# Kernel optimization log

Hardware: AMD Instinct MI355X
Metric: run time of the kernel (lower is better)

## Reference

```python
import jax, jax.numpy as jnp
import numpy as np

P = 8  # patch size hardcoded in FSAS/DFFN
EPS = 1e-5


def conv1x1(x, w):
    # x: [B,C,H,W], w: [Cout,Cin]
    return jnp.einsum('bchw,oc->bohw', x, w)


def dwconv3(x, w):
    # depthwise 3x3, w: [C,1,3,3]
    return jax.lax.conv_general_dilated(
        x, w, window_strides=(1, 1), padding='SAME',
        dimension_numbers=('NCHW', 'OIHW', 'NCHW'),
        feature_group_count=x.shape[1])


def layernorm_c(x, w, b):
    # WithBias LayerNorm over channel dim (torch: b c h w -> b (h w) c, LN over c)
    mu = jnp.mean(x, axis=1, keepdims=True)
    var = jnp.var(x, axis=1, keepdims=True)
    return (x - mu) / jnp.sqrt(var + EPS) * w[None, :, None, None] + b[None, :, None, None]


def to_patches(x):
    # [B,C,H,W] -> [B,C,H/P,W/P,P,P]
    B, C, H, W = x.shape
    return x.reshape(B, C, H // P, P, W // P, P).transpose(0, 1, 2, 4, 3, 5)


def from_patches(xp):
    B, C, h, w, p1, p2 = xp.shape
    return xp.transpose(0, 1, 2, 4, 3, 5).reshape(B, C, h * p1, w * p2)


def fsas(x, w_hidden, dw, norm_w, norm_b, w_out):
    hidden = conv1x1(x, w_hidden)          # [B,6d,H,W]
    qkv = dwconv3(hidden, dw)
    q, k, v = jnp.split(qkv, 3, axis=1)    # each [B,2d,H,W]
    qf = jnp.fft.rfft2(to_patches(q))
    kf = jnp.fft.rfft2(to_patches(k))
    out = jnp.fft.irfft2(qf * kf, s=(P, P))
    out = layernorm_c(from_patches(out), norm_w, norm_b)
    return conv1x1(v * out, w_out)


def dffn(x, w_in, fft_w, dw, w_out):
    x = conv1x1(x, w_in)                   # [B,2h,H,W]
    xf = jnp.fft.rfft2(to_patches(x))
    # fft_w: [2h,1,1,P,P//2+1] broadcasts against [B,2h,h,w,P,P//2+1]
    x = from_patches(jnp.fft.irfft2(xf * fft_w, s=(P, P)))
    x1, x2 = jnp.split(dwconv3(x, dw), 2, axis=1)
    return conv1x1(jax.nn.gelu(x1, approximate=False) * x2, w_out)


def setup_inputs() -> dict:
    key = jax.random.key(0)
    ks = jax.random.split(key, 10)
    d = 48
    h = int(d * 3)  # ffn_expansion_factor=3 -> hidden_features=144
    B, H, W = 2, 256, 256

    def n(k, shape, s=0.05):
        return jax.random.normal(k, shape, jnp.float32) * s

    return {
        'x': jax.random.normal(ks[0], (B, d, H, W), jnp.float32),
        'norm1_w': jnp.ones((d,), jnp.float32),
        'norm1_b': jnp.zeros((d,), jnp.float32),
        'attn_w_hidden': n(ks[1], (6 * d, d)),
        'attn_dw': n(ks[2], (6 * d, 1, 3, 3), 0.2),
        'attn_norm_w': jnp.ones((2 * d,), jnp.float32),
        'attn_norm_b': jnp.zeros((2 * d,), jnp.float32),
        'attn_w_out': n(ks[3], (d, 2 * d)),
        'norm2_w': jnp.ones((d,), jnp.float32),
        'norm2_b': jnp.zeros((d,), jnp.float32),
        'ffn_w_in': n(ks[4], (2 * h, d)),
        'ffn_fft': 1.0 + n(ks[5], (2 * h, 1, 1, P, P // 2 + 1), 0.1),
        'ffn_dw': n(ks[6], (2 * h, 1, 3, 3), 0.2),
        'ffn_w_out': n(ks[7], (d, h)),
    }


def reference(x, norm1_w, norm1_b, attn_w_hidden, attn_dw, attn_norm_w,
              attn_norm_b, attn_w_out, norm2_w, norm2_b, ffn_w_in, ffn_fft,
              ffn_dw, ffn_w_out):
    x = x + fsas(layernorm_c(x, norm1_w, norm1_b),
                 attn_w_hidden, attn_dw, attn_norm_w, attn_norm_b, attn_w_out)
    x = x + dffn(layernorm_c(x, norm2_w, norm2_b),
                 ffn_w_in, ffn_fft, ffn_dw, ffn_w_out)
    return x
```

## Files before the change

### kernel.cpp

```cpp
#include <hip/hip_runtime.h>
#include <hip/hip_bf16.h>
#include <cstddef>


constexpr int HWC = 65536;

typedef short short8 __attribute__((ext_vector_type(8)));
typedef __bf16 bf16x8 __attribute__((ext_vector_type(8)));
typedef float f32x4 __attribute__((ext_vector_type(4)));

__device__ inline unsigned short f2bf(float f) {
  __hip_bfloat16 h = __float2bfloat16(f);
  return *reinterpret_cast<unsigned short*>(&h);
}
__device__ inline float bf2f(unsigned short u) {
  __hip_bfloat16 h;
  *reinterpret_cast<unsigned short*>(&h) = u;
  return __bfloat162float(h);
}

union V8 { uint4 v; unsigned short us[8]; short s[8]; };

__device__ inline void load8f(const unsigned short* p, float* f) {
  V8 u; u.v = *reinterpret_cast<const uint4*>(p);
#pragma unroll
  for (int j = 0; j < 8; j++) f[j] = bf2f(u.us[j]);
}
__device__ inline void store8bf(unsigned short* p, const float* f) {
  V8 u;
#pragma unroll
  for (int j = 0; j < 8; j++) u.us[j] = f2bf(f[j]);
  *reinterpret_cast<uint4*>(p) = u.v;
}

__device__ inline void fdft8(const float* x, float* e) {
  const float c = 0.70710678118654752f;
  float t0 = x[0] + x[4], t1 = x[0] - x[4];
  float t2 = x[2] + x[6], t3 = x[2] - x[6];
  float t4 = x[1] + x[5], t5 = x[1] - x[5];
  float t6 = x[3] + x[7], t7 = x[3] - x[7];
  float A = c * (t5 - t7), B = c * (t5 + t7);
  float s1 = t0 + t2, s2 = t4 + t6;
  e[0] = s1 + s2;
  e[7] = s1 - s2;
  e[1] = t1 + A;
  e[5] = t1 - A;
  e[2] = -(B + t3);
  e[6] = t3 - B;
  e[3] = t0 - t2;
  e[4] = t6 - t4;
}

__global__ __launch_bounds__(64) void k_prep_w(
    const float* __restrict__ awh, const float* __restrict__ awo,
    const float* __restrict__ fwi, const float* __restrict__ fwo,
    unsigned short* __restrict__ wp) {
  int row = blockIdx.x, t = threadIdx.x;
  const float* src; int K, KP; unsigned short* dst;
  if (row < 288)      { src = awh + row * 48;        K = 48;  KP = 64;
                        dst = wp + row * 64; }
  else if (row < 336) { int r = row - 288; src = awo + r * 96; K = 96; KP = 96;
                        dst = wp + 18432 + r * 96; }
  else if (row < 624) { int r = row - 336; src = fwi + r * 48; K = 48; KP = 64;
                        dst = wp + 23040 + r * 64; }
  else                { int r = row - 624; src = fwo + r * 144; K = 144; KP = 160;
                        dst = wp + 41472 + r * 160; }
  for (int k = t; k < KP; k += 64) dst[k] = f2bf(k < K ? src[k] : 0.f);
}

template <int M, int K, int KP, int XF, int EPI>
__global__ __launch_bounds__(256) void k_gemm(
    const unsigned short* __restrict__ wb, const void* __restrict__ s1,
    const unsigned short* __restrict__ s2, const float* __restrict__ lnw,
    const float* __restrict__ lnb, const void* __restrict__ res,
    void* __restrict__ out) {
  constexpr int STRIDE = KP + 8;
  constexpr int KS = KP / 32;
  constexpr int NT = (M + 63) / 64;
  __shared__ __align__(16) short Xs[64 * STRIDE];
  __shared__ __align__(16) short Vs[(XF == 2) ? 64 * STRIDE : 4];
  __shared__ float redS[4][64], redS2[4][64], mus[64], invs[64];

  int tid = threadIdx.x;
  unsigned bid = blockIdx.x;
  int b = (int)(bid >> 10);
  int hw0 = (int)(bid & 1023) * 64;

  if (XF == 1) {
    const float* xp = (const float*)s1 + (size_t)b * 48 * HWC + hw0;
    for (int idx = tid; idx < 48 * 16; idx += 256) {
      int c = idx >> 4, colg = (idx & 15) * 4;
      float4 f = *reinterpret_cast<const float4*>(xp + (size_t)c * HWC + colg);
      Xs[(colg + 0) * STRIDE + c] = (short)f2bf(f.x);
      Xs[(colg + 1) * STRIDE + c] = (short)f2bf(f.y);
      Xs[(colg + 2) * STRIDE + c] = (short)f2bf(f.z);
      Xs[(colg + 3) * STRIDE + c] = (short)f2bf(f.w);
    }
  } else if (XF == 2) {
    const unsigned short* up =
        (const unsigned short*)s1 + (size_t)b * 96 * HWC + hw0;
    const unsigned short* vp = s2 + ((size_t)(b * 288 + 192)) * HWC + hw0;
    for (int idx = tid; idx < 96 * 16; idx += 256) {
      int c = idx >> 4, colg = (idx & 15) * 4;
      ushort4 uv = *reinterpret_cast<const ushort4*>(up + (size_t)c * HWC + colg);
      Xs[(colg + 0) * STRIDE + c] = (short)uv.x;
      Xs[(colg + 1) * STRIDE + c] = (short)uv.y;
      Xs[(colg + 2) * STRIDE + c] = (short)uv.z;
      Xs[(colg + 3) * STRIDE + c] = (short)uv.w;
      ushort4 vv = *reinterpret_cast<const ushort4*>(vp + (size_t)c * HWC + colg);
      Vs[(colg + 0) * STRIDE + c] = (short)vv.x;
      Vs[(colg + 1) * STRIDE + c] = (short)vv.y;
      Vs[(colg + 2) * STRIDE + c] = (short)vv.z;
      Vs[(colg + 3) * STRIDE + c] = (short)vv.w;
    }
  } else if (XF == 3) {
    const unsigned short* xp =
        (const unsigned short*)s1 + (size_t)b * 48 * HWC + hw0;
    for (int idx = tid; idx < 48 * 16; idx += 256) {
      int c = idx >> 4, colg = (idx & 15) * 4;
      ushort4 uv = *reinterpret_cast<const ushort4*>(xp + (size_t)c * HWC + colg);
      Xs[(colg + 0) * STRIDE + c] = (short)uv.x;
      Xs[(colg + 1) * STRIDE + c] = (short)uv.y;
      Xs[(colg + 2) * STRIDE + c] = (short)uv.z;
      Xs[(colg + 3) * STRIDE + c] = (short)uv.w;
    }
  } else {
    const unsigned short* p1 =
        (const unsigned short*)s1 + (size_t)b * 96 * HWC + hw0;
    const unsigned short* p2 = s2 + (size_t)b * 48 * HWC + hw0;
    for (int idx = tid; idx < K * 16; idx += 256) {
      int c = idx >> 4, colg = (idx & 15) * 4;
      const unsigned short* p =
          (c < 96) ? (p1 + (size_t)c * HWC + colg)
                   : (p2 + (size_t)(c - 96) * HWC + colg);
      ushort4 uv = *reinterpret_cast<const ushort4*>(p);
      Xs[(colg + 0) * STRIDE + c] = (short)uv.x;
      Xs[(colg + 1) * STRIDE + c] = (short)uv.y;
      Xs[(colg + 2) * STRIDE + c] = (short)uv.z;
      Xs[(colg + 3) * STRIDE + c] = (short)uv.w;
    }
  }

  if constexpr (KP > K) {
    constexpr int PAD = KP - K;
    for (int idx = tid; idx < 64 * PAD; idx += 256) {
      int col = idx / PAD, c = K + (idx % PAD);
      Xs[col * STRIDE + c] = 0;
    }
  }

  if (XF != 0) {
    constexpr int KC = (XF == 2) ? 96 : 48;
    __syncthreads();
    {
      int col = tid & 63, q = tid >> 6;
      float s = 0.f, s2 = 0.f;
      for (int c = q * (KC / 4); c < (q + 1) * (KC / 4); c++) {
        float v = bf2f((unsigned short)Xs[col * STRIDE + c]);
        s += v; s2 += v * v;
      }
      redS[q][col] = s; redS2[q][col] = s2;
    }
    __syncthreads();
    if (tid < 64) {
      float ss = redS[0][tid] + redS[1][tid] + redS[2][tid] + redS[3][tid];
      float ss2 = redS2[0][tid] + redS2[1][tid] + redS2[2][tid] + redS2[3][tid];
      float mu = ss * (1.f / KC);
      float var = ss2 * (1.f / KC) - mu * mu;
      mus[tid] = mu; invs[tid] = rsqrtf(var + 1e-5f);
    }
    __syncthreads();
    for (int idx = tid; idx < KC * 64; idx += 256) {
      int c = idx >> 6, col = idx & 63;
      float v = bf2f((unsigned short)Xs[col * STRIDE + c]);
      v = (v - mus[col]) * invs[col] * lnw[c] + lnb[c];
      if (XF == 2) v *= bf2f((unsigned short)Vs[col * STRIDE + c]);
      Xs[col * STRIDE + c] = (short)f2bf(v);
    }
  }
  __syncthreads();

  int lane = tid & 63, wvi = tid >> 6;
  int quad = lane >> 4, mc = lane & 15;
  int kbase = quad * 8;

  short8 bfr[4][KS];
#pragma unroll
  for (int ns = 0; ns < 4; ns++)
#pragma unroll
    for (int ks = 0; ks < KS; ks++)
      bfr[ns][ks] = *reinterpret_cast<const short8*>(
          Xs + (ns * 16 + mc) * STRIDE + ks * 32 + kbase);

  short* Es = Xs;
#pragma unroll
  for (int t = 0; t < NT; t++) {
    int mb = (wvi + 4 * t) * 16;
    f32x4 accs[4];
    if (mb < M) {
      short8 afr[KS];
#pragma unroll
      for (int ks = 0; ks < KS; ks++)
        afr[ks] = *reinterpret_cast<const short8*>(
            wb + (size_t)(mb + mc) * KP + ks * 32 + kbase);
#pragma unroll
      for (int ns = 0; ns < 4; ns++) {
        f32x4 acc = {0.f, 0.f, 0.f, 0.f};
#pragma unroll
        for (int ks = 0; ks < KS; ks++)
          acc = __builtin_amdgcn_mfma_f32_16x16x32_bf16(
              __builtin_bit_cast(bf16x8, afr[ks]),
              __builtin_bit_cast(bf16x8, bfr[ns][ks]), acc, 0, 0, 0);
        accs[ns] = acc;
      }
    }
    __syncthreads();
    if (mb < M) {
      int chl = wvi * 16 + quad * 4;
#pragma unroll
      for (int ns = 0; ns < 4; ns++)
#pragma unroll
        for (int r = 0; r < 4; r++)
          Es[(chl + r) * 72 + ns * 16 + mc] = (short)f2bf(accs[ns][r]);
    }
    __syncthreads();
#pragma unroll
    for (int i = 0; i < 2; i++) {
      int chl = (tid >> 3) + 32 * i;
      int px0 = (tid & 7) * 8;
      int m = 64 * t + chl;
      if (m < M) {
        V8 ev;
        ev.v = *reinterpret_cast<const uint4*>(Es + chl * 72 + px0);
        size_t off = ((size_t)(b * ((EPI == 0) ? M : 48) + m)) * HWC + hw0 + px0;
        if (EPI == 0) {
          *reinterpret_cast<uint4*>((unsigned short*)out + off) = ev.v;
        } else if (EPI == 1) {
          const float* rp = (const float*)res + off;
          float4 ra = *reinterpret_cast<const float4*>(rp);
          float4 rb = *reinterpret_cast<const float4*>(rp + 4);
          V8 pk;
          pk.us[0] = f2bf(ra.x + bf2f(ev.us[0]));
          pk.us[1] = f2bf(ra.y + bf2f(ev.us[1]));
          pk.us[2] = f2bf(ra.z + bf2f(ev.us[2]));
          pk.us[3] = f2bf(ra.w + bf2f(ev.us[3]));
          pk.us[4] = f2bf(rb.x + bf2f(ev.us[4]));
          pk.us[5] = f2bf(rb.y + bf2f(ev.us[5]));
          pk.us[6] = f2bf(rb.z + bf2f(ev.us[6]));
          pk.us[7] = f2bf(rb.w + bf2f(ev.us[7]));
          *reinterpret_cast<uint4*>((unsigned short*)out + off) = pk.v;
        } else {
          V8 rv;
          rv.v = *reinterpret_cast<const uint4*>((const unsigned short*)res + off);
          float* op = (float*)out + off;
          float4 oa, ob;
          oa.x = bf2f(rv.us[0]) + bf2f(ev.us[0]);
          oa.y = bf2f(rv.us[1]) + bf2f(ev.us[1]);
          oa.z = bf2f(rv.us[2]) + bf2f(ev.us[2]);
          oa.w = bf2f(rv.us[3]) + bf2f(ev.us[3]);
          ob.x = bf2f(rv.us[4]) + bf2f(ev.us[4]);
          ob.y = bf2f(rv.us[5]) + bf2f(ev.us[5]);
          ob.z = bf2f(rv.us[6]) + bf2f(ev.us[6]);
          ob.w = bf2f(rv.us[7]) + bf2f(ev.us[7]);
          *reinterpret_cast<float4*>(op) = oa;
          *reinterpret_cast<float4*>(op + 4) = ob;
        }
      }
    }
  }
}

__global__ __launch_bounds__(256) void k_dwconv3v(
    const unsigned short* __restrict__ in, const float* __restrict__ dw,
    unsigned short* __restrict__ out) {
  int tid = threadIdx.x;
  unsigned bid = blockIdx.x;
  int y0 = (int)(bid & 31) * 8;
  unsigned t = bid >> 5;
  int c = 192 + (int)(t % 96u);
  int b = (int)(t / 96u);
  const unsigned short* ip = in + ((size_t)(b * 288 + c)) * HWC;
  float wv[9];
#pragma unroll
  for (int k = 0; k < 9; k++) wv[k] = dw[c * 9 + k];
  int r = tid >> 5, seg = tid & 31, lane = tid & 63;
  int y = y0 + r;
  float f[3][8];
#pragma unroll
  for (int dy = 0; dy < 3; dy++) {
    int yy = y + dy - 1;
    if (yy >= 0 && yy < 256) {
      load8f(ip + yy * 256 + seg * 8, f[dy]);
    } else {
#pragma unroll
      for (int j = 0; j < 8; j++) f[dy][j] = 0.f;
    }
  }
  float o[8];
#pragma unroll
  for (int dy = 0; dy < 3; dy++) {
    float lv = __shfl(f[dy][7], lane - 1, 64);
    float rv = __shfl(f[dy][0], lane + 1, 64);
    if (seg == 0) lv = 0.f;
    if (seg == 31) rv = 0.f;
#pragma unroll
    for (int j = 0; j < 8; j++) {
      float xl = (j == 0) ? lv : f[dy][j - 1];
      float xr = (j == 7) ? rv : f[dy][j + 1];
      float v = xl * wv[dy * 3] + f[dy][j] * wv[dy * 3 + 1] + xr * wv[dy * 3 + 2];
      o[j] = (dy == 0) ? v : o[j] + v;
    }
  }
  store8bf(out + ((size_t)(b * 288 + c)) * HWC + y * 256 + seg * 8, o);
}

__global__ __launch_bounds__(256) void k_fsas_fused(
    const unsigned short* __restrict__ hid, const float* __restrict__ dw,
    unsigned short* __restrict__ out) {
  constexpr int LSTR = 260;
  __shared__ __align__(16) float qs[8 * LSTR];
  __shared__ __align__(16) float kt[8 * LSTR];
  int tid = threadIdx.x;
  unsigned bid = blockIdx.x;
  int py = (int)(bid & 31);
  int c = (int)((bid >> 5) % 96u);
  int b = (int)((bid >> 5) / 96u);
  const unsigned short* qp = hid + ((size_t)(b * 288 + c)) * HWC;
  const unsigned short* kp = hid + ((size_t)(b * 288 + 96 + c)) * HWC;
  float w1[9], w2[9];
#pragma unroll
  for (int k = 0; k < 9; k++) {
    w1[k] = dw[c * 9 + k];
    w2[k] = dw[(96 + c) * 9 + k];
  }
  int r = tid >> 5, seg = tid & 31, lane = tid & 63;
  int y = py * 8 + r;
  float f1[3][8], f2[3][8];
#pragma unroll
  for (int dy = 0; dy < 3; dy++) {
    int yy = y + dy - 1;
    if (yy >= 0 && yy < 256) {
      load8f(qp + yy * 256 + seg * 8, f1[dy]);
      load8f(kp + yy * 256 + seg * 8, f2[dy]);
    } else {
#pragma unroll
      for (int j = 0; j < 8; j++) { f1[dy][j] = 0.f; f2[dy][j] = 0.f; }
    }
  }
  float d1[8], d2[8];
#pragma unroll
  for (int j = 0; j < 8; j++) { d1[j] = 0.f; d2[j] = 0.f; }
#pragma unroll
  for (int dy = 0; dy < 3; dy++) {
    float lv1 = __shfl(f1[dy][7], lane - 1, 64);
    float rv1 = __shfl(f1[dy][0], lane + 1, 64);
    float lv2 = __shfl(f2[dy][7], lane - 1, 64);
    float rv2 = __shfl(f2[dy][0], lane + 1, 64);
    if (seg == 0) { lv1 = 0.f; lv2 = 0.f; }
    if (seg == 31) { rv1 = 0.f; rv2 = 0.f; }
#pragma unroll
    for (int j = 0; j < 8; j++) {
      float xl1 = (j == 0) ? lv1 : f1[dy][j - 1];
      float xr1 = (j == 7) ? rv1 : f1[dy][j + 1];
      float xl2 = (j == 0) ? lv2 : f2[dy][j - 1];
      float xr2 = (j == 7) ? rv2 : f2[dy][j + 1];
      d1[j] += xl1 * w1[dy * 3] + f1[dy][j] * w1[dy * 3 + 1] + xr1 * w1[dy * 3 + 2];
      d2[j] += xl2 * w2[dy * 3] + f2[dy][j] * w2[dy * 3 + 1] + xr2 * w2[dy * 3 + 2];
    }
  }
  {
    float e1[8], e2[8];
    fdft8(d1, e1);
    fdft8(d2, e2);
    float4 a1 = {e1[0], e1[1], e1[2], e1[3]};
    float4 b1 = {e1[4], e1[5], e1[6], e1[7]};
    float4 a2 = {e2[0], e2[1], e2[2], e2[3]};
    float4 b2 = {e2[4], e2[5], e2[6], e2[7]};
    *reinterpret_cast<float4*>(&qs[r * LSTR + seg * 8]) = a1;
    *reinterpret_cast<float4*>(&qs[r * LSTR + seg * 8 + 4]) = b1;
    *reinterpret_cast<float4*>(&kt[r * LSTR + seg * 8]) = a2;
    *reinterpret_cast<float4*>(&kt[r * LSTR + seg * 8 + 4]) = b2;
  }
  __syncthreads();
  int p = tid >> 3, a = tid & 7;
  float Z[8];
#pragma unroll
  for (int j = 0; j < 8; j++) Z[j] = 0.f;
#pragma unroll
  for (int i = 0; i < 8; i++) {
    float4 qa = *reinterpret_cast<const float4*>(&qs[i * LSTR + p * 8]);
    float4 qb = *reinterpret_cast<const float4*>(&qs[i * LSTR + p * 8 + 4]);
    int ar = (a - i) & 7;
    float4 ka = *reinterpret_cast<const float4*>(&kt[ar * LSTR + p * 8]);
    float4 kb = *reinterpret_cast<const float4*>(&kt[ar * LSTR + p * 8 + 4]);
    Z[0] += qa.x * ka.x;
    Z[7] += qb.w * kb.w;
    Z[1] += qa.y * ka.y - qa.z * ka.z;
    Z[2] += qa.y * ka.z + qa.z * ka.y;
    Z[3] += qa.w * ka.w - qb.x * kb.x;
    Z[4] += qa.w * kb.x + qb.x * ka.w;
    Z[5] += qb.y * kb.y - qb.z * kb.z;
    Z[6] += qb.y * kb.z + qb.z * kb.y;
  }
  float acc[8];
  {
    const float c2 = 0.70710678118654752f;
    float Z0 = Z[0], Z1r = Z[1], Z1i = Z[2], Z2r = Z[3];
    float Z2i = Z[4], Z3r = Z[5], Z3i = Z[6], Z4 = Z[7];
    float u0 = Z0 + Z4, u1 = Z0 - Z4;
    float E = 2.f * Z2r, F = 2.f * (Z1r + Z3r), G = 2.f * (Z1i - Z3i);
    float T = 2.f * Z2i;
    float P = 2.f * c2 * (Z1r - Z1i), Qv = 2.f * c2 * (Z1r + Z1i);
    float R = 2.f * c2 * (Z3r + Z3i), S = 2.f * c2 * (Z3r - Z3i);
    acc[0] = 0.125f * (u0 + E + F);
    acc[4] = 0.125f * (u0 + E - F);
    acc[2] = 0.125f * (u0 - E - G);
    acc[6] = 0.125f * (u0 - E + G);
    acc[1] = 0.125f * (u1 + P - T - R);
    acc[3] = 0.125f * (u1 - Qv + T + S);
    acc[5] = 0.125f * (u1 - P - T + R);
    acc[7] = 0.125f * (u1 + Qv + T - S);
  }
  store8bf(out + ((size_t)(b * 96 + c)) * HWC + (py * 8 + a) * 256 + p * 8,
           acc);
}

__device__ const float c_cos8[8] = {
    1.f, 0.70710678118654752f, 0.f, -0.70710678118654752f,
    -1.f, -0.70710678118654752f, 0.f, 0.70710678118654752f};

__global__ __launch_bounds__(64) void k_make_cmat(
    const float* __restrict__ fftw, unsigned short* __restrict__ cmat) {
  __shared__ float sf[64];
  int c = blockIdx.x;
  int a = threadIdx.x >> 3, b2 = threadIdx.x & 7;
  const float* W = fftw + c * 40;
  float acc = 0.f;
  for (int u = 0; u < 8; u++) {
    for (int v = 0; v < 8; v++) {
      float wv;
      if (v <= 4) {
        if (v == 0 || v == 4)
          wv = 0.5f * (W[u * 5 + v] + W[((8 - u) & 7) * 5 + v]);
        else
          wv = W[u * 5 + v];
      } else {
        wv = W[((8 - u) & 7) * 5 + (8 - v)];
      }
      acc += wv * c_cos8[(u * a + v * b2) & 7];
    }
  }
  sf[threadIdx.x] = acc * (1.f / 64.f);
  __syncthreads();
  unsigned short* cp = cmat + (size_t)c * 4096 + threadIdx.x * 64;
  for (int k8 = 0; k8 < 64; k8 += 8) {
    float v[8];
    int ka = k8 >> 3;
    int ia = ((a - ka) & 7) * 8;
#pragma unroll
    for (int j = 0; j < 8; j++) v[j] = sf[ia + ((b2 - j) & 7)];
    store8bf(cp + k8, v);
  }
}

__global__ __launch_bounds__(256) void k_patchconv_mfma(
    unsigned short* y, const unsigned short* __restrict__ cmat) {
  __shared__ __align__(16) short Bs[32 * 72];
  __shared__ __align__(16) short As[64 * 72];
  int tid = threadIdx.x;
  unsigned bid = blockIdx.x;
  int py = (int)(bid & 31);
  int c = (int)((bid >> 5) % 288u);
  int b = (int)((bid >> 5) / 288u);
  unsigned short* yp = y + ((size_t)(b * 288 + c)) * HWC + py * 2048;
  {
    int rr = tid >> 5, seg = tid & 31;
    *reinterpret_cast<uint4*>(Bs + seg * 72 + rr * 8) =
        *reinterpret_cast<const uint4*>(yp + rr * 256 + seg * 8);
  }
  {
    const unsigned short* cp = cmat + (size_t)c * 4096;
    int m = tid >> 2, kq = (tid & 3) * 16;
    *reinterpret_cast<uint4*>(As + m * 72 + kq) =
        *reinterpret_cast<const uint4*>(cp + m * 64 + kq);
    *reinterpret_cast<uint4*>(As + m * 72 + kq + 8) =
        *reinterpret_cast<const uint4*>(cp + m * 64 + kq + 8);
  }
  __syncthreads();
  int lane = tid & 63, wvi = tid >> 6;
  int quad = lane >> 4, mc = lane & 15;
  int kbase = quad * 8;
  short8 afr[2];
#pragma unroll
  for (int ks = 0; ks < 2; ks++)
    afr[ks] = *reinterpret_cast<const short8*>(
        As + (wvi * 16 + mc) * 72 + ks * 32 + kbase);
#pragma unroll
  for (int nt = 0; nt < 2; nt++) {
    short8 bfr[2];
#pragma unroll
    for (int ks = 0; ks < 2; ks++)
      bfr[ks] = *reinterpret_cast<const short8*>(
          Bs + (nt * 16 + mc) * 72 + ks * 32 + kbase);
    f32x4 acc = {0.f, 0.f, 0.f, 0.f};
#pragma unroll
    for (int ks = 0; ks < 2; ks++)
      acc = __builtin_amdgcn_mfma_f32_16x16x32_bf16(
          __builtin_bit_cast(bf16x8, afr[ks]),
          __builtin_bit_cast(bf16x8, bfr[ks]), acc, 0, 0, 0);
    int p = nt * 16 + mc;
    int m0 = wvi * 16 + quad * 4;
    int a = m0 >> 3, b8 = m0 & 7;
    ushort4 pk;
    pk.x = f2bf(acc[0]); pk.y = f2bf(acc[1]);
    pk.z = f2bf(acc[2]); pk.w = f2bf(acc[3]);
    *reinterpret_cast<ushort4*>(yp + a * 256 + p * 8 + b8) = pk;
  }
}

__global__ __launch_bounds__(256) void k_ffn_gate(
    const unsigned short* __restrict__ z, const float* __restrict__ dwf,
    unsigned short* __restrict__ g1, unsigned short* __restrict__ g2) {
  int tid = threadIdx.x;
  unsigned bid = blockIdx.x;
  int y0 = (int)(bid & 31) * 8;
  unsigned t = bid >> 5;
  int c = (int)(t % 144u);
  int b = (int)(t / 144u);
  const unsigned short* zp1 = z + ((size_t)(b * 288 + c)) * HWC;
  const unsigned short* zp2 = z + ((size_t)(b * 288 + 144 + c)) * HWC;
  float w1[9], w2[9];
#pragma unroll
  for (int k = 0; k < 9; k++) {
    w1[k] = dwf[c * 9 + k];
    w2[k] = dwf[(144 + c) * 9 + k];
  }
  int r = tid >> 5, seg = tid & 31, lane = tid & 63;
  int y = y0 + r;
  float f1[3][8], f2[3][8];
#pragma unroll
  for (int dy = 0; dy < 3; dy++) {
    int yy = y + dy - 1;
    if (yy >= 0 && yy < 256) {
      load8f(zp1 + yy * 256 + seg * 8, f1[dy]);
      load8f(zp2 + yy * 256 + seg * 8, f2[dy]);
    } else {
#pragma unroll
      for (int j = 0; j < 8; j++) { f1[dy][j] = 0.f; f2[dy][j] = 0.f; }
    }
  }
  float d1[8], d2[8];
#pragma unroll
  for (int j = 0; j < 8; j++) { d1[j] = 0.f; d2[j] = 0.f; }
#pragma unroll
  for (int dy = 0; dy < 3; dy++) {
    float lv1 = __shfl(f1[dy][7], lane - 1, 64);
    float rv1 = __shfl(f1[dy][0], lane + 1, 64);
    float lv2 = __shfl(f2[dy][7], lane - 1, 64);
    float rv2 = __shfl(f2[dy][0], lane + 1, 64);
    if (seg == 0) { lv1 = 0.f; lv2 = 0.f; }
    if (seg == 31) { rv1 = 0.f; rv2 = 0.f; }
#pragma unroll
    for (int j = 0; j < 8; j++) {
      float xl1 = (j == 0) ? lv1 : f1[dy][j - 1];
      float xr1 = (j == 7) ? rv1 : f1[dy][j + 1];
      float xl2 = (j == 0) ? lv2 : f2[dy][j - 1];
      float xr2 = (j == 7) ? rv2 : f2[dy][j + 1];
      d1[j] += xl1 * w1[dy * 3] + f1[dy][j] * w1[dy * 3 + 1] + xr1 * w1[dy * 3 + 2];
      d2[j] += xl2 * w2[dy * 3] + f2[dy][j] * w2[dy * 3 + 1] + xr2 * w2[dy * 3 + 2];
    }
  }
  float o[8];
#pragma unroll
  for (int j = 0; j < 8; j++)
    o[j] = 0.5f * d1[j] * (1.f + erff(d1[j] * 0.70710678118654752f)) * d2[j];
  unsigned short* gp = (c < 96)
      ? g1 + ((size_t)(b * 96 + c)) * HWC
      : g2 + ((size_t)(b * 48 + (c - 96))) * HWC;
  store8bf(gp + y * 256 + seg * 8, o);
}

extern "C" void kernel_launch(void* const* d_in, const int* in_sizes, int n_in,
                              void* d_out, int out_size, void* d_ws,
                              size_t ws_size, hipStream_t stream) {
  (void)in_sizes; (void)n_in; (void)out_size; (void)ws_size;
  const float* x   = (const float*)d_in[0];
  const float* n1w = (const float*)d_in[1];
  const float* n1b = (const float*)d_in[2];
  const float* awh = (const float*)d_in[3];
  const float* adw = (const float*)d_in[4];
  const float* anw = (const float*)d_in[5];
  const float* anb = (const float*)d_in[6];
  const float* awo = (const float*)d_in[7];
  const float* n2w = (const float*)d_in[8];
  const float* n2b = (const float*)d_in[9];
  const float* fwi = (const float*)d_in[10];
  const float* fff = (const float*)d_in[11];
  const float* fdw = (const float*)d_in[12];
  const float* fwo = (const float*)d_in[13];

  unsigned short* QKV  = (unsigned short*)d_ws;
  unsigned short* HID  = (unsigned short*)((char*)d_ws + 75497472);
  unsigned short* U    = (unsigned short*)((char*)d_ws + 150994944);
  unsigned short* X1   = (unsigned short*)((char*)d_ws + 176160768);
  unsigned short* G2   = (unsigned short*)((char*)d_ws + 188743680);
  unsigned short* CMAT = G2;
  unsigned short* WP   = (unsigned short*)((char*)d_ws + 201326592);
  unsigned short* WA = WP;
  unsigned short* WO = WP + 18432;
  unsigned short* WI = WP + 23040;
  unsigned short* WF = WP + 41472;

  k_prep_w<<<672, 64, 0, stream>>>(awh, awo, fwi, fwo, WP);
  k_make_cmat<<<288, 64, 0, stream>>>(fff, CMAT);
  k_gemm<288, 48, 64, 1, 0><<<2048, 256, 0, stream>>>(WA, x, nullptr, n1w,
                                                      n1b, nullptr, HID);
  k_dwconv3v<<<2 * 96 * 32, 256, 0, stream>>>(HID, adw, QKV);
  k_fsas_fused<<<2 * 96 * 32, 256, 0, stream>>>(HID, adw, U);
  k_gemm<48, 96, 96, 2, 1><<<2048, 256, 0, stream>>>(WO, U, QKV, anw, anb, x,
                                                     X1);
  k_gemm<288, 48, 64, 3, 0><<<2048, 256, 0, stream>>>(WI, X1, nullptr, n2w,
                                                      n2b, nullptr, QKV);
  k_patchconv_mfma<<<2 * 288 * 32, 256, 0, stream>>>(QKV, CMAT);
  k_ffn_gate<<<2 * 144 * 32, 256, 0, stream>>>(QKV, fdw, U, G2);
  k_gemm<48, 144, 160, 0, 2><<<2048, 256, 0, stream>>>(WF, U, G2, nullptr,
                                                       nullptr, X1,
                                                       (float*)d_out);
}
```

Measured before the change: 291.7 us.

## Fuse DFFN patch spectral filter with gated dwconv and merge v-dwconv into FSAS

Replaces the DFFN patch-convolution MFMA kernel and the separate gate kernel with one fused kernel. It forward-DFTs rows of each 8x8 patch into shared memory (fp16), applies the filter as a circulant row convolution in frequency space, inverse-DFTs, and then runs the 3x3 depthwise conv with GELU gating from shared memory, recomputing halo patch rows. This removes the write and re-read of the filtered 288-channel tensor and one launch. The standalone v-path dwconv is folded into the FSAS kernel grid as extra blocks, and filter-matrix prep moves into the weight-prep kernel. Costs are halo recompute of neighbouring patches, fp16 intermediate precision, and heavier per-block shared memory.

```diff
diff --git a/kernel.cpp b/kernel.cpp
--- a/kernel.cpp
+++ b/kernel.cpp
@@ -8,6 +8,7 @@
 typedef short short8 __attribute__((ext_vector_type(8)));
 typedef __bf16 bf16x8 __attribute__((ext_vector_type(8)));
 typedef float f32x4 __attribute__((ext_vector_type(4)));
+typedef _Float16 f16x8 __attribute__((ext_vector_type(8)));
 
 __device__ inline unsigned short f2bf(float f) {
   __hip_bfloat16 h = __float2bfloat16(f);
@@ -51,11 +52,55 @@
   e[4] = t6 - t4;
 }
 
+__device__ inline void idft8(const float* Z, float* acc) {
+  const float c2 = 0.70710678118654752f;
+  float Z0 = Z[0], Z1r = Z[1], Z1i = Z[2], Z2r = Z[3];
+  float Z2i = Z[4], Z3r = Z[5], Z3i = Z[6], Z4 = Z[7];
+  float u0 = Z0 + Z4, u1 = Z0 - Z4;
+  float E = 2.f * Z2r, F = 2.f * (Z1r + Z3r), G = 2.f * (Z1i - Z3i);
+  float T = 2.f * Z2i;
+  float P = 2.f * c2 * (Z1r - Z1i), Qv = 2.f * c2 * (Z1r + Z1i);
+  float R = 2.f * c2 * (Z3r + Z3i), S = 2.f * c2 * (Z3r - Z3i);
+  acc[0] = 0.125f * (u0 + E + F);
+  acc[4] = 0.125f * (u0 + E - F);
+  acc[2] = 0.125f * (u0 - E - G);
+  acc[6] = 0.125f * (u0 - E + G);
+  acc[1] = 0.125f * (u1 + P - T - R);
+  acc[3] = 0.125f * (u1 - Qv + T + S);
+  acc[5] = 0.125f * (u1 - P - T + R);
+  acc[7] = 0.125f * (u1 + Qv + T - S);
+}
+
+__device__ const float c_cos8[8] = {
+    1.f, 0.70710678118654752f, 0.f, -0.70710678118654752f,
+    -1.f, -0.70710678118654752f, 0.f, 0.70710678118654752f};
+__device__ const float c_sin8[8] = {
+    0.f, 0.70710678118654752f, 1.f, 0.70710678118654752f,
+    0.f, -0.70710678118654752f, -1.f, -0.70710678118654752f};
+
 __global__ __launch_bounds__(64) void k_prep_w(
     const float* __restrict__ awh, const float* __restrict__ awo,
     const float* __restrict__ fwi, const float* __restrict__ fwo,
-    unsigned short* __restrict__ wp) {
+    const float* __restrict__ fftw, unsigned short* __restrict__ wp,
+    float* __restrict__ srow) {
   int row = blockIdx.x, t = threadIdx.x;
+  if (row >= 672) {
+    int c = row - 672;
+    const float* W = fftw + c * 40;
+    int j = t >> 3, bin = t & 7;
+    int v = (bin + 1) >> 1;
+    int im = (bin != 0) && ((bin & 1) == 0);
+    float acc = 0.f;
+    for (int u = 0; u < 8; u++) {
+      float wv = (v == 0 || v == 4)
+                     ? 0.5f * (W[u * 5 + v] + W[((8 - u) & 7) * 5 + v])
+                     : W[u * 5 + v];
+      int ph = (u * j) & 7;
+      acc += wv * (im ? c_sin8[ph] : c_cos8[ph]);
+    }
+    srow[c * 64 + j * 8 + bin] = 0.125f * acc;
+    return;
+  }
   const float* src; int K, KP; unsigned short* dst;
   if (row < 288)      { src = awh + row * 48;        K = 48;  KP = 64;
                         dst = wp + row * 64; }
@@ -270,61 +315,58 @@
   }
 }
 
-__global__ __launch_bounds__(256) void k_dwconv3v(
-    const unsigned short* __restrict__ in, const float* __restrict__ dw,
-    unsigned short* __restrict__ out) {
-  int tid = threadIdx.x;
-  unsigned bid = blockIdx.x;
-  int y0 = (int)(bid & 31) * 8;
-  unsigned t = bid >> 5;
-  int c = 192 + (int)(t % 96u);
-  int b = (int)(t / 96u);
-  const unsigned short* ip = in + ((size_t)(b * 288 + c)) * HWC;
-  float wv[9];
-#pragma unroll
-  for (int k = 0; k < 9; k++) wv[k] = dw[c * 9 + k];
-  int r = tid >> 5, seg = tid & 31, lane = tid & 63;
-  int y = y0 + r;
-  float f[3][8];
-#pragma unroll
-  for (int dy = 0; dy < 3; dy++) {
-    int yy = y + dy - 1;
-    if (yy >= 0 && yy < 256) {
-      load8f(ip + yy * 256 + seg * 8, f[dy]);
-    } else {
-#pragma unroll
-      for (int j = 0; j < 8; j++) f[dy][j] = 0.f;
-    }
-  }
-  float o[8];
-#pragma unroll
-  for (int dy = 0; dy < 3; dy++) {
-    float lv = __shfl(f[dy][7], lane - 1, 64);
-    float rv = __shfl(f[dy][0], lane + 1, 64);
-    if (seg == 0) lv = 0.f;
-    if (seg == 31) rv = 0.f;
-#pragma unroll
-    for (int j = 0; j < 8; j++) {
-      float xl = (j == 0) ? lv : f[dy][j - 1];
-      float xr = (j == 7) ? rv : f[dy][j + 1];
-      float v = xl * wv[dy * 3] + f[dy][j] * wv[dy * 3 + 1] + xr * wv[dy * 3 + 2];
-      o[j] = (dy == 0) ? v : o[j] + v;
-    }
-  }
-  store8bf(out + ((size_t)(b * 288 + c)) * HWC + y * 256 + seg * 8, o);
-}
-
 __global__ __launch_bounds__(256) void k_fsas_fused(
     const unsigned short* __restrict__ hid, const float* __restrict__ dw,
-    unsigned short* __restrict__ out) {
+    unsigned short* __restrict__ out, unsigned short* __restrict__ qkv) {
   constexpr int LSTR = 260;
   __shared__ __align__(16) float qs[8 * LSTR];
   __shared__ __align__(16) float kt[8 * LSTR];
   int tid = threadIdx.x;
   unsigned bid = blockIdx.x;
   int py = (int)(bid & 31);
-  int c = (int)((bid >> 5) % 96u);
-  int b = (int)((bid >> 5) / 96u);
+  unsigned t = bid >> 5;
+  int cc = (int)(t % 192u);
+  int b = (int)(t / 192u);
+  int r = tid >> 5, seg = tid & 31, lane = tid & 63;
+
+  if (cc >= 96) {
+    int c = 96 + cc;
+    const unsigned short* ip = hid + ((size_t)(b * 288 + c)) * HWC;
+    float wv[9];
+#pragma unroll
+    for (int k = 0; k < 9; k++) wv[k] = dw[c * 9 + k];
+    int y = py * 8 + r;
+    float f[3][8];
+#pragma unroll
+    for (int dy = 0; dy < 3; dy++) {
+      int yy = y + dy - 1;
+      if (yy >= 0 && yy < 256) {
+        load8f(ip + yy * 256 + seg * 8, f[dy]);
+      } else {
+#pragma unroll
+        for (int j = 0; j < 8; j++) f[dy][j] = 0.f;
+      }
+    }
+    float o[8];
+#pragma unroll
+    for (int dy = 0; dy < 3; dy++) {
+      float lv = __shfl(f[dy][7], lane - 1, 64);
+      float rv = __shfl(f[dy][0], lane + 1, 64);
+      if (seg == 0) lv = 0.f;
+      if (seg == 31) rv = 0.f;
+#pragma unroll
+      for (int j = 0; j < 8; j++) {
+        float xl = (j == 0) ? lv : f[dy][j - 1];
+        float xr = (j == 7) ? rv : f[dy][j + 1];
+        float v = xl * wv[dy * 3] + f[dy][j] * wv[dy * 3 + 1] + xr * wv[dy * 3 + 2];
+        o[j] = (dy == 0) ? v : o[j] + v;
+      }
+    }
+    store8bf(qkv + ((size_t)(b * 288 + c)) * HWC + y * 256 + seg * 8, o);
+    return;
+  }
+
+  int c = cc;
   const unsigned short* qp = hid + ((size_t)(b * 288 + c)) * HWC;
   const unsigned short* kp = hid + ((size_t)(b * 288 + 96 + c)) * HWC;
   float w1[9], w2[9];
@@ -333,7 +375,6 @@
     w1[k] = dw[c * 9 + k];
     w2[k] = dw[(96 + c) * 9 + k];
   }
-  int r = tid >> 5, seg = tid & 31, lane = tid & 63;
   int y = py * 8 + r;
   float f1[3][8], f2[3][8];
 #pragma unroll
@@ -403,181 +444,146 @@
     Z[6] += qb.y * kb.z + qb.z * kb.y;
   }
   float acc[8];
-  {
-    const float c2 = 0.70710678118654752f;
-    float Z0 = Z[0], Z1r = Z[1], Z1i = Z[2], Z2r = Z[3];
-    float Z2i = Z[4], Z3r = Z[5], Z3i = Z[6], Z4 = Z[7];
-    float u0 = Z0 + Z4, u1 = Z0 - Z4;
-    float E = 2.f * Z2r, F = 2.f * (Z1r + Z3r), G = 2.f * (Z1i - Z3i);
-    float T = 2.f * Z2i;
-    float P = 2.f * c2 * (Z1r - Z1i), Qv = 2.f * c2 * (Z1r + Z1i);
-    float R = 2.f * c2 * (Z3r + Z3i), S = 2.f * c2 * (Z3r - Z3i);
-    acc[0] = 0.125f * (u0 + E + F);
-    acc[4] = 0.125f * (u0 + E - F);
-    acc[2] = 0.125f * (u0 - E - G);
-    acc[6] = 0.125f * (u0 - E + G);
-    acc[1] = 0.125f * (u1 + P - T - R);
-    acc[3] = 0.125f * (u1 - Qv + T + S);
-    acc[5] = 0.125f * (u1 - P - T + R);
-    acc[7] = 0.125f * (u1 + Qv + T - S);
-  }
+  idft8(Z, acc);
   store8bf(out + ((size_t)(b * 96 + c)) * HWC + (py * 8 + a) * 256 + p * 8,
            acc);
 }
 
-__device__ const float c_cos8[8] = {
-    1.f, 0.70710678118654752f, 0.f, -0.70710678118654752f,
-    -1.f, -0.70710678118654752f, 0.f, 0.70710678118654752f};
-
-__global__ __launch_bounds__(64) void k_make_cmat(
-    const float* __restrict__ fftw, unsigned short* __restrict__ cmat) {
-  __shared__ float sf[64];
-  int c = blockIdx.x;
-  int a = threadIdx.x >> 3, b2 = threadIdx.x & 7;
-  const float* W = fftw + c * 40;
-  float acc = 0.f;
-  for (int u = 0; u < 8; u++) {
-    for (int v = 0; v < 8; v++) {
-      float wv;
-      if (v <= 4) {
-        if (v == 0 || v == 4)
-          wv = 0.5f * (W[u * 5 + v] + W[((8 - u) & 7) * 5 + v]);
-        else
-          wv = W[u * 5 + v];
-      } else {
-        wv = W[((8 - u) & 7) * 5 + (8 - v)];
-      }
-      acc += wv * c_cos8[(u * a + v * b2) & 7];
-    }
-  }
-  sf[threadIdx.x] = acc * (1.f / 64.f);
-  __syncthreads();
-  unsigned short* cp = cmat + (size_t)c * 4096 + threadIdx.x * 64;
-  for (int k8 = 0; k8 < 64; k8 += 8) {
-    float v[8];
-    int ka = k8 >> 3;
-    int ia = ((a - ka) & 7) * 8;
-#pragma unroll
-    for (int j = 0; j < 8; j++) v[j] = sf[ia + ((b2 - j) & 7)];
-    store8bf(cp + k8, v);
-  }
-}
-
-__global__ __launch_bounds__(256) void k_patchconv_mfma(
-    unsigned short* y, const unsigned short* __restrict__ cmat) {
-  __shared__ __align__(16) short Bs[32 * 72];
-  __shared__ __align__(16) short As[64 * 72];
+__device__ inline void zrow_accum(const _Float16* spect, const float* S8,
+                                  int base, int a, int p, float* acc) {
+  float Z[8];
+#pragma unroll
+  for (int j = 0; j < 8; j++) Z[j] = 0.f;
+#pragma unroll
+  for (int i = 0; i < 8; i++) {
+    f16x8 qv = *reinterpret_cast<const f16x8*>(&spect[(base + i) * 264 + p * 8]);
+    const float* S = S8 + (((a - i) & 7) << 3);
+    float4 sa = *reinterpret_cast<const float4*>(S);
+    float4 sc = *reinterpret_cast<const float4*>(S + 4);
+    float q0 = (float)qv[0], q1 = (float)qv[1], q2 = (float)qv[2];
+    float q3 = (float)qv[3], q4 = (float)qv[4], q5 = (float)qv[5];
+    float q6 = (float)qv[6], q7 = (float)qv[7];
+    Z[0] += q0 * sa.x;
+    Z[1] += q1 * sa.y - q2 * sa.z;
+    Z[2] += q1 * sa.z + q2 * sa.y;
+    Z[3] += q3 * sa.w - q4 * sc.x;
+    Z[4] += q3 * sc.x + q4 * sa.w;
+    Z[5] += q5 * sc.y - q6 * sc.z;
+    Z[6] += q5 * sc.z + q6 * sc.y;
+    Z[7] += q7 * sc.w;
+  }
+  idft8(Z, acc);
+}
+
+__global__ __launch_bounds__(256) void k_dffn_fused(
+    const unsigned short* __restrict__ y, const float* __restrict__ srow,
+    const float* __restrict__ dwf, unsigned short* __restrict__ g1,
+    unsigned short* __restrict__ g2) {
+  constexpr int SSTR = 264;
+  constexpr int ZSTR = 264;
+  __shared__ __align__(16) _Float16 spect[24 * SSTR];
+  __shared__ __align__(16) _Float16 zb[2][10 * ZSTR];
+  __shared__ float sb[2][64];
   int tid = threadIdx.x;
   unsigned bid = blockIdx.x;
   int py = (int)(bid & 31);
-  int c = (int)((bid >> 5) % 288u);
-  int b = (int)((bid >> 5) / 288u);
-  unsigned short* yp = y + ((size_t)(b * 288 + c)) * HWC + py * 2048;
-  {
-    int rr = tid >> 5, seg = tid & 31;
-    *reinterpret_cast<uint4*>(Bs + seg * 72 + rr * 8) =
-        *reinterpret_cast<const uint4*>(yp + rr * 256 + seg * 8);
-  }
-  {
-    const unsigned short* cp = cmat + (size_t)c * 4096;
-    int m = tid >> 2, kq = (tid & 3) * 16;
-    *reinterpret_cast<uint4*>(As + m * 72 + kq) =
-        *reinterpret_cast<const uint4*>(cp + m * 64 + kq);
-    *reinterpret_cast<uint4*>(As + m * 72 + kq + 8) =
-        *reinterpret_cast<const uint4*>(cp + m * 64 + kq + 8);
+  int cg = (int)((bid >> 5) % 144u);
+  int b  = (int)((bid >> 5) / 144u);
+  int y0 = py * 8;
+  if (tid < 128) {
+    int h = tid >> 6, t = tid & 63;
+    sb[h][t] = srow[(cg + h * 144) * 64 + t];
+  }
+#pragma unroll
+  for (int h = 0; h < 2; h++) {
+    const unsigned short* yp = y + ((size_t)(b * 288 + cg + h * 144)) * HWC;
+    __syncthreads();
+#pragma unroll
+    for (int pass = 0; pass < 3; pass++) {
+      int unit = pass * 8 + (tid >> 5);
+      int slab = py - 1 + (unit >> 3);
+      int rr = unit & 7, seg = tid & 31;
+      float d[8];
+      if (slab >= 0 && slab < 32) {
+        load8f(yp + (slab * 8 + rr) * 256 + seg * 8, d);
+      } else {
+#pragma unroll
+        for (int j = 0; j < 8; j++) d[j] = 0.f;
+      }
+      float e[8];
+      fdft8(d, e);
+      f16x8 ev;
+#pragma unroll
+      for (int j = 0; j < 8; j++) ev[j] = (_Float16)e[j];
+      *reinterpret_cast<f16x8*>(&spect[unit * SSTR + seg * 8]) = ev;
+    }
+    __syncthreads();
+    {
+      int p = tid >> 3, a = tid & 7;
+      float acc[8];
+      zrow_accum(spect, &sb[h][0], 8, a, p, acc);
+      f16x8 zv;
+#pragma unroll
+      for (int j = 0; j < 8; j++) zv[j] = (_Float16)acc[j];
+      *reinterpret_cast<f16x8*>(&zb[h][(1 + a) * ZSTR + p * 8]) = zv;
+    }
+    if (tid < 64) {
+      int p = tid >> 1, hs = tid & 1;
+      float acc[8];
+      zrow_accum(spect, &sb[h][0], hs ? 16 : 0, hs ? 0 : 7, p, acc);
+      f16x8 zv;
+#pragma unroll
+      for (int j = 0; j < 8; j++) zv[j] = (_Float16)acc[j];
+      *reinterpret_cast<f16x8*>(&zb[h][(hs ? 9 : 0) * ZSTR + p * 8]) = zv;
+    }
   }
   __syncthreads();
-  int lane = tid & 63, wvi = tid >> 6;
-  int quad = lane >> 4, mc = lane & 15;
-  int kbase = quad * 8;
-  short8 afr[2];
-#pragma unroll
-  for (int ks = 0; ks < 2; ks++)
-    afr[ks] = *reinterpret_cast<const short8*>(
-        As + (wvi * 16 + mc) * 72 + ks * 32 + kbase);
-#pragma unroll
-  for (int nt = 0; nt < 2; nt++) {
-    short8 bfr[2];
-#pragma unroll
-    for (int ks = 0; ks < 2; ks++)
-      bfr[ks] = *reinterpret_cast<const short8*>(
-          Bs + (nt * 16 + mc) * 72 + ks * 32 + kbase);
-    f32x4 acc = {0.f, 0.f, 0.f, 0.f};
-#pragma unroll
-    for (int ks = 0; ks < 2; ks++)
-      acc = __builtin_amdgcn_mfma_f32_16x16x32_bf16(
-          __builtin_bit_cast(bf16x8, afr[ks]),
-          __builtin_bit_cast(bf16x8, bfr[ks]), acc, 0, 0, 0);
-    int p = nt * 16 + mc;
-    int m0 = wvi * 16 + quad * 4;
-    int a = m0 >> 3, b8 = m0 & 7;
-    ushort4 pk;
-    pk.x = f2bf(acc[0]); pk.y = f2bf(acc[1]);
-    pk.z = f2bf(acc[2]); pk.w = f2bf(acc[3]);
-    *reinterpret_cast<ushort4*>(yp + a * 256 + p * 8 + b8) = pk;
-  }
-}
-
-__global__ __launch_bounds__(256) void k_ffn_gate(
-    const unsigned short* __restrict__ z, const float* __restrict__ dwf,
-    unsigned short* __restrict__ g1, unsigned short* __restrict__ g2) {
-  int tid = threadIdx.x;
-  unsigned bid = blockIdx.x;
-  int y0 = (int)(bid & 31) * 8;
-  unsigned t = bid >> 5;
-  int c = (int)(t % 144u);
-  int b = (int)(t / 144u);
-  const unsigned short* zp1 = z + ((size_t)(b * 288 + c)) * HWC;
-  const unsigned short* zp2 = z + ((size_t)(b * 288 + 144 + c)) * HWC;
+  int r = tid >> 5, seg = tid & 31;
   float w1[9], w2[9];
 #pragma unroll
   for (int k = 0; k < 9; k++) {
-    w1[k] = dwf[c * 9 + k];
-    w2[k] = dwf[(144 + c) * 9 + k];
-  }
-  int r = tid >> 5, seg = tid & 31, lane = tid & 63;
-  int y = y0 + r;
-  float f1[3][8], f2[3][8];
+    w1[k] = dwf[cg * 9 + k];
+    w2[k] = dwf[(144 + cg) * 9 + k];
+  }
+  float d1[8], d2[8];
+#pragma unroll
+  for (int j = 0; j < 8; j++) { d1[j] = 0.f; d2[j] = 0.f; }
 #pragma unroll
   for (int dy = 0; dy < 3; dy++) {
-    int yy = y + dy - 1;
-    if (yy >= 0 && yy < 256) {
-      load8f(zp1 + yy * 256 + seg * 8, f1[dy]);
-      load8f(zp2 + yy * 256 + seg * 8, f2[dy]);
-    } else {
-#pragma unroll
-      for (int j = 0; j < 8; j++) { f1[dy][j] = 0.f; f2[dy][j] = 0.f; }
-    }
-  }
-  float d1[8], d2[8];
-#pragma unroll
-  for (int j = 0; j < 8; j++) { d1[j] = 0.f; d2[j] = 0.f; }
-#pragma unroll
-  for (int dy = 0; dy < 3; dy++) {
-    float lv1 = __shfl(f1[dy][7], lane - 1, 64);
-    float rv1 = __shfl(f1[dy][0], lane + 1, 64);
-    float lv2 = __shfl(f2[dy][7], lane - 1, 64);
-    float rv2 = __shfl(f2[dy][0], lane + 1, 64);
-    if (seg == 0) { lv1 = 0.f; lv2 = 0.f; }
-    if (seg == 31) { rv1 = 0.f; rv2 = 0.f; }
-#pragma unroll
-    for (int j = 0; j < 8; j++) {
-      float xl1 = (j == 0) ? lv1 : f1[dy][j - 1];
-      float xr1 = (j == 7) ? rv1 : f1[dy][j + 1];
-      float xl2 = (j == 0) ? lv2 : f2[dy][j - 1];
-      float xr2 = (j == 7) ? rv2 : f2[dy][j + 1];
-      d1[j] += xl1 * w1[dy * 3] + f1[dy][j] * w1[dy * 3 + 1] + xr1 * w1[dy * 3 + 2];
-      d2[j] += xl2 * w2[dy * 3] + f2[dy][j] * w2[dy * 3 + 1] + xr2 * w2[dy * 3 + 2];
+    int zr = r + dy;
+    {
+      const _Float16* z = &zb[0][zr * ZSTR];
+      f16x8 cv = *reinterpret_cast<const f16x8*>(&z[seg * 8]);
+      float lv = (seg == 0) ? 0.f : (float)z[seg * 8 - 1];
+      float rv = (seg == 31) ? 0.f : (float)z[seg * 8 + 8];
+#pragma unroll
+      for (int j = 0; j < 8; j++) {
+        float xl = (j == 0) ? lv : (float)cv[j - 1];
+        float xr = (j == 7) ? rv : (float)cv[j + 1];
+        d1[j] += xl * w1[dy * 3] + (float)cv[j] * w1[dy * 3 + 1] + xr * w1[dy * 3 + 2];
+      }
+    }
+    {
+      const _Float16* z = &zb[1][zr * ZSTR];
+      f16x8 cv = *reinterpret_cast<const f16x8*>(&z[seg * 8]);
+      float lv = (seg == 0) ? 0.f : (float)z[seg * 8 - 1];
+      float rv = (seg == 31) ? 0.f : (float)z[seg * 8 + 8];
+#pragma unroll
+      for (int j = 0; j < 8; j++) {
+        float xl = (j == 0) ? lv : (float)cv[j - 1];
+        float xr = (j == 7) ? rv : (float)cv[j + 1];
+        d2[j] += xl * w2[dy * 3] + (float)cv[j] * w2[dy * 3 + 1] + xr * w2[dy * 3 + 2];
+      }
     }
   }
   float o[8];
 #pragma unroll
   for (int j = 0; j < 8; j++)
     o[j] = 0.5f * d1[j] * (1.f + erff(d1[j] * 0.70710678118654752f)) * d2[j];
-  unsigned short* gp = (c < 96)
-      ? g1 + ((size_t)(b * 96 + c)) * HWC
-      : g2 + ((size_t)(b * 48 + (c - 96))) * HWC;
-  store8bf(gp + y * 256 + seg * 8, o);
+  unsigned short* gp = (cg < 96)
+      ? g1 + ((size_t)(b * 96 + cg)) * HWC
+      : g2 + ((size_t)(b * 48 + (cg - 96))) * HWC;
+  store8bf(gp + (y0 + r) * 256 + seg * 8, o);
 }
 
 extern "C" void kernel_launch(void* const* d_in, const int* in_sizes, int n_in,
@@ -604,25 +610,22 @@
   unsigned short* U    = (unsigned short*)((char*)d_ws + 150994944);
   unsigned short* X1   = (unsigned short*)((char*)d_ws + 176160768);
   unsigned short* G2   = (unsigned short*)((char*)d_ws + 188743680);
-  unsigned short* CMAT = G2;
   unsigned short* WP   = (unsigned short*)((char*)d_ws + 201326592);
+  float*          SROW = (float*)((char*)d_ws + 201424896);
   unsigned short* WA = WP;
   unsigned short* WO = WP + 18432;
   unsigned short* WI = WP + 23040;
   unsigned short* WF = WP + 41472;
 
-  k_prep_w<<<672, 64, 0, stream>>>(awh, awo, fwi, fwo, WP);
-  k_make_cmat<<<288, 64, 0, stream>>>(fff, CMAT);
+  k_prep_w<<<960, 64, 0, stream>>>(awh, awo, fwi, fwo, fff, WP, SROW);
   k_gemm<288, 48, 64, 1, 0><<<2048, 256, 0, stream>>>(WA, x, nullptr, n1w,
                                                       n1b, nullptr, HID);
-  k_dwconv3v<<<2 * 96 * 32, 256, 0, stream>>>(HID, adw, QKV);
-  k_fsas_fused<<<2 * 96 * 32, 256, 0, stream>>>(HID, adw, U);
+  k_fsas_fused<<<2 * 192 * 32, 256, 0, stream>>>(HID, adw, U, QKV);
   k_gemm<48, 96, 96, 2, 1><<<2048, 256, 0, stream>>>(WO, U, QKV, anw, anb, x,
                                                      X1);
   k_gemm<288, 48, 64, 3, 0><<<2048, 256, 0, stream>>>(WI, X1, nullptr, n2w,
                                                       n2b, nullptr, QKV);
-  k_patchconv_mfma<<<2 * 288 * 32, 256, 0, stream>>>(QKV, CMAT);
-  k_ffn_gate<<<2 * 144 * 32, 256, 0, stream>>>(QKV, fdw, U, G2);
+  k_dffn_fused<<<2 * 144 * 32, 256, 0, stream>>>(QKV, SROW, fdw, U, G2);
   k_gemm<48, 144, 160, 0, 2><<<2048, 256, 0, stream>>>(WF, U, G2, nullptr,
                                                        nullptr, X1,
                                                        (float*)d_out);
```

Result: slower. 361.0 us (+23.8%).
